# Performance work log

Measured on AMD Instinct MI355X. Metric: run time of the kernel, lower is better.

The kernel has to match this reference:

```python
import jax, jax.numpy as jnp
import numpy as np

NUM_HEADS = 4
NUM_GROUPS = 8
EPS = 1e-5


def setup_inputs() -> dict:
    key = jax.random.key(0)
    ks = jax.random.split(key, 5)
    B, C, H, W = 16, 512, 32, 32
    s = 1.0 / np.sqrt(C)
    return {
        "x": jax.random.normal(ks[0], (B, C, H, W), dtype=jnp.float32),
        "norm_w": jnp.ones((C,), jnp.float32),
        "norm_b": jnp.zeros((C,), jnp.float32),
        "q_w": jax.random.normal(ks[1], (C, C), jnp.float32) * s,
        "q_b": jnp.zeros((C,), jnp.float32),
        "k_w": jax.random.normal(ks[2], (C, C), jnp.float32) * s,
        "k_b": jnp.zeros((C,), jnp.float32),
        "v_w": jax.random.normal(ks[3], (C, C), jnp.float32) * s,
        "v_b": jnp.zeros((C,), jnp.float32),
        "p_w": jax.random.normal(ks[4], (C, C), jnp.float32) * s,
        "p_b": jnp.zeros((C,), jnp.float32),
    }


def _group_norm(x, w, b):
    # x: (B, C, N) -> GroupNorm over (C//G, N) per group
    B, C, N = x.shape
    g = x.reshape(B, NUM_GROUPS, C // NUM_GROUPS, N)
    mean = g.mean(axis=(2, 3), keepdims=True)
    var = g.var(axis=(2, 3), keepdims=True)
    g = (g - mean) * jax.lax.rsqrt(var + EPS)
    x = g.reshape(B, C, N)
    return x * w[None, :, None] + b[None, :, None]


def reference(x, norm_w, norm_b, q_w, q_b, k_w, k_b, v_w, v_b, p_w, p_b):
    B, C, H, W = x.shape
    N = H * W
    Ch = C // NUM_HEADS  # channels per head
    h = _group_norm(x.reshape(B, C, N), norm_w, norm_b)
    # 1x1 Conv1d == channel matmul: (o c, b c n -> b o n)
    q = jnp.einsum('oc,bcn->bon', q_w, h) + q_b[None, :, None]
    k = jnp.einsum('oc,bcn->bon', k_w, h) + k_b[None, :, None]
    v = jnp.einsum('oc,bcn->bon', v_w, h) + v_b[None, :, None]
    q = q.reshape(B, NUM_HEADS, Ch, N)
    k = k.reshape(B, NUM_HEADS, Ch, N)
    v = v.reshape(B, NUM_HEADS, Ch, N)
    attn = jnp.einsum('bhcn,bhcm->bhnm', q, k) * (1.0 / np.sqrt(Ch))
    attn = jax.nn.softmax(attn, axis=-1)
    out = jnp.einsum('bhnm,bhcm->bhcn', attn, v).reshape(B, C, N)
    out = jnp.einsum('oc,bcn->bon', p_w, out) + p_b[None, :, None]
    return x + out.reshape(B, C, H, W)
```

## Files before the change

kernel.cpp:

```cpp
#include <hip/hip_runtime.h>
#include <hip/hip_bf16.h>
#include <math.h>

#define B_    16
#define C_    512
#define N_    1024
#define G_    8
#define HEADS 4
#define CH    128
#define EPS   1e-5f

typedef __attribute__((ext_vector_type(8))) short short8;
typedef __attribute__((ext_vector_type(4))) float f32x4;
typedef __attribute__((ext_vector_type(16))) float f32x16;
typedef __attribute__((ext_vector_type(4))) int i32x4;

__device__ __forceinline__ unsigned short f2bf(float f) {
  union { float f; unsigned int i; } x; x.f = f;
  unsigned int r = x.i + 0x7FFFu + ((x.i >> 16) & 1u);
  return (unsigned short)(r >> 16);
}

__global__ __launch_bounds__(256) void gn_stats(const float* __restrict__ x,
                                                float* __restrict__ stats) {
  int bg = blockIdx.x;
  const float4* p4 = (const float4*)(x + (size_t)bg * (C_ / G_) * N_);
  const int n4 = (C_ / G_) * N_ / 4;
  float s = 0.f, ss = 0.f;
  for (int i = threadIdx.x; i < n4; i += 256) {
    float4 v = p4[i];
    s  += v.x + v.y + v.z + v.w;
    ss += v.x * v.x + v.y * v.y + v.z * v.z + v.w * v.w;
  }
  for (int o = 32; o; o >>= 1) { s += __shfl_down(s, o); ss += __shfl_down(ss, o); }
  __shared__ float ls[4], lss[4];
  int wid = threadIdx.x >> 6, lane = threadIdx.x & 63;
  if (lane == 0) { ls[wid] = s; lss[wid] = ss; }
  __syncthreads();
  if (threadIdx.x == 0) {
    float S = ls[0] + ls[1] + ls[2] + ls[3];
    float SS = lss[0] + lss[1] + lss[2] + lss[3];
    const float inv = 1.f / ((C_ / G_) * N_);
    float mean = S * inv;
    float var = SS * inv - mean * mean;
    stats[bg * 2]     = mean;
    stats[bg * 2 + 1] = rsqrtf(var + EPS);
  }
}

__global__ __launch_bounds__(256) void conv_w(const float* __restrict__ q, const float* __restrict__ k,
                                              const float* __restrict__ v, const float* __restrict__ p,
                                              unsigned short* __restrict__ dst) {
  const int n = C_ * C_;
  int i = blockIdx.x * 256 + threadIdx.x;
  if (i < n) {
    dst[i]         = f2bf(q[i]);
    dst[n + i]     = f2bf(k[i]);
    dst[2 * n + i] = f2bf(v[i]);
    dst[3 * n + i] = f2bf(p[i]);
  }
}

__global__ __launch_bounds__(256) void gn_apply(const float* __restrict__ x,
                                                const float* __restrict__ stats,
                                                const float* __restrict__ gw,
                                                const float* __restrict__ gb,
                                                unsigned short* __restrict__ hT) {
  __shared__ float T[64][65];
  int b = blockIdx.z, c0 = blockIdx.y * 64, n0 = blockIdx.x * 64;
  int g = c0 / (C_ / G_);
  float mean = stats[(b * G_ + g) * 2], rstd = stats[(b * G_ + g) * 2 + 1];
  int t = threadIdx.x;
  for (int it = 0; it < 4; it++) {
    int L = it * 256 + t;
    int cc = L >> 4, nf = L & 15;
    float4 v = *(const float4*)&x[((size_t)b * C_ + c0 + cc) * N_ + n0 + nf * 4];
    float sw = gw[c0 + cc] * rstd, sb = gb[c0 + cc] - mean * sw;
    T[cc][nf * 4 + 0] = v.x * sw + sb;
    T[cc][nf * 4 + 1] = v.y * sw + sb;
    T[cc][nf * 4 + 2] = v.z * sw + sb;
    T[cc][nf * 4 + 3] = v.w * sw + sb;
  }
  __syncthreads();
  for (int it = 0; it < 4; it++) {
    int L = it * 256 + t;
    int nn = L >> 4, cv = L & 15;
    ushort4 o;
    o.x = f2bf(T[cv * 4 + 0][nn]);
    o.y = f2bf(T[cv * 4 + 1][nn]);
    o.z = f2bf(T[cv * 4 + 2][nn]);
    o.w = f2bf(T[cv * 4 + 3][nn]);
    *(ushort4*)&hT[((size_t)b * N_ + n0 + nn) * C_ + c0 + cv * 4] = o;
  }
}

template <bool OUT_BF16, bool BIAS_I, bool RESID>
__global__ __launch_bounds__(256) void gemm_tn(const unsigned short* __restrict__ A,
                                               const unsigned short* __restrict__ Bt,
                                               const float* __restrict__ bias,
                                               const float* __restrict__ resid,
                                               void* __restrict__ out,
                                               int M, int Ncols, int K,
                                               long aBS, long bBS, long oBS) {
  __shared__ __align__(16) unsigned short As[128][72];
  __shared__ __align__(16) unsigned short Bs[128][72];
  int b = blockIdx.z;
  const unsigned short* Ab = A + (size_t)b * aBS;
  const unsigned short* Bb = Bt + (size_t)b * bBS;
  int i0 = blockIdx.y * 128, j0 = blockIdx.x * 128;
  int t = threadIdx.x;
  int w = t >> 6, l = t & 63;
  int wi = (w >> 1) * 64, wj = (w & 1) * 64;
  int lr = l & 15, lk = (l >> 4) * 8;

  f32x4 acc[4][4];
  const f32x4 zf = {0.f, 0.f, 0.f, 0.f};
#pragma unroll
  for (int m = 0; m < 4; m++)
#pragma unroll
    for (int n = 0; n < 4; n++) acc[m][n] = zf;

  for (int kt = 0; kt < K; kt += 64) {
    __syncthreads();
#pragma unroll
    for (int it = 0; it < 4; it++) {
      int L = it * 256 + t;
      int row = L >> 3, c8 = (L & 7) * 8;
      *(uint4*)&As[row][c8] = *(const uint4*)&Ab[(size_t)(i0 + row) * K + kt + c8];
      *(uint4*)&Bs[row][c8] = *(const uint4*)&Bb[(size_t)(j0 + row) * K + kt + c8];
    }
    __syncthreads();
#pragma unroll
    for (int ks = 0; ks < 64; ks += 32) {
      short8 af[4], bf[4];
#pragma unroll
      for (int m = 0; m < 4; m++) af[m] = *(const short8*)&As[wi + m * 16 + lr][ks + lk];
#pragma unroll
      for (int n = 0; n < 4; n++) bf[n] = *(const short8*)&Bs[wj + n * 16 + lr][ks + lk];
#pragma unroll
      for (int m = 0; m < 4; m++)
#pragma unroll
        for (int n = 0; n < 4; n++)
          acc[m][n] = __builtin_amdgcn_mfma_f32_16x16x32_bf16(af[m], bf[n], acc[m][n], 0, 0, 0);
    }
  }

  int rbase = (l >> 4) * 4;
#pragma unroll
  for (int m = 0; m < 4; m++) {
    int ig = i0 + wi + m * 16 + rbase;
#pragma unroll
    for (int n = 0; n < 4; n++) {
      int jg = j0 + wj + n * 16 + lr;
#pragma unroll
      for (int r = 0; r < 4; r++) {
        float vv = acc[m][n][r];
        vv += BIAS_I ? bias[ig + r] : bias[jg];
        size_t oidx = (size_t)b * oBS + (size_t)(ig + r) * Ncols + jg;
        if (RESID) vv += resid[oidx];
        if (OUT_BF16) ((unsigned short*)out)[oidx] = f2bf(vv);
        else ((float*)out)[oidx] = vv;
      }
    }
  }
}

__global__ __launch_bounds__(512, 2) void attn_kernel(const unsigned short* __restrict__ qT,
                                                      const unsigned short* __restrict__ kT,
                                                      const unsigned short* __restrict__ v,
                                                      unsigned short* __restrict__ aoT) {
  __shared__ __align__(16) unsigned short Ks[2][64 * 128];
  __shared__ __align__(16) unsigned short Vs[2][128 * 64];
  const int t = threadIdx.x, w = t >> 6, l = t & 63;
  const int h = l >> 5, l31 = l & 31, l7 = l & 7;
  const int bh = blockIdx.y, b = bh >> 2, hd = bh & 3, c0h = hd * CH;
  const int qg = blockIdx.x * 256 + w * 32 + l31;
  const float sc2 = 0.08838834764831845f * 1.4426950408889634f;
  const float THRRAW = 11.5f / sc2;

  short8 qf[8];
  const unsigned short* qrow = qT + ((size_t)b * N_ + qg) * C_ + c0h;
#pragma unroll
  for (int kc = 0; kc < 8; kc++)
    qf[kc] = *(const short8*)&qrow[kc * 16 + h * 8];

  f32x16 o[4];
#pragma unroll
  for (int ct = 0; ct < 4; ct++) o[ct] = (f32x16)(0.f);
  float m = -INFINITY, lsum = 0.f;

  auto stage = [&](int cur, int tt) {
    int mt = tt * 64;
#pragma unroll
    for (int i = 0; i < 2; i++) {
      int seg = w * 2 + i;
      {
        int row = seg * 4 + (l >> 4);
        int gc = (l & 15) ^ (row & 7);
        const unsigned short* src = kT + ((size_t)b * N_ + mt + row) * C_ + c0h + gc * 8;
        __builtin_amdgcn_global_load_lds((const __attribute__((address_space(1))) void*)src,
                                         (__attribute__((address_space(3))) void*)&Ks[cur][seg * 512],
                                         16, 0, 0);
      }
      {
        int row = seg * 8 + (l >> 3);
        int gc = (l & 7) ^ (row & 7);
        const unsigned short* src = v + ((size_t)b * C_ + c0h + row) * N_ + mt + gc * 8;
        __builtin_amdgcn_global_load_lds((const __attribute__((address_space(1))) void*)src,
                                         (__attribute__((address_space(3))) void*)&Vs[cur][seg * 512],
                                         16, 0, 0);
      }
    }
  };

  stage(0, 0);

  for (int tt = 0; tt < 16; tt++) {
    int cur = tt & 1;
    __syncthreads();
    if (tt < 15) stage(cur ^ 1, tt + 1);

    f32x16 st0 = (f32x16)(0.f), st1 = (f32x16)(0.f);
    const unsigned short* KsB = &Ks[cur][0];
    __builtin_amdgcn_s_setprio(1);
#pragma unroll
    for (int kc = 0; kc < 8; kc++) {
      short8 kf0 = *(const short8*)&KsB[l31 * 128 + (((2 * kc + h) ^ l7) * 8)];
      short8 kf1 = *(const short8*)&KsB[(32 + l31) * 128 + (((2 * kc + h) ^ l7) * 8)];
      st0 = __builtin_amdgcn_mfma_f32_32x32x16_bf16(kf0, qf[kc], st0, 0, 0, 0);
      st1 = __builtin_amdgcn_mfma_f32_32x32x16_bf16(kf1, qf[kc], st1, 0, 0, 0);
    }
    __builtin_amdgcn_s_setprio(0);

    float pmax = st0[0];
#pragma unroll
    for (int r = 1; r < 16; r++) pmax = fmaxf(pmax, st0[r]);
#pragma unroll
    for (int r = 0; r < 16; r++) pmax = fmaxf(pmax, st1[r]);
    pmax = fmaxf(pmax, __shfl_xor(pmax, 32));

    bool defer = (pmax <= m + THRRAW);
    bool skip = __all(defer);
    float mnew = skip ? m : fmaxf(m, pmax);
    float alpha = skip ? 1.f : exp2f((m - mnew) * sc2);
    float mb = mnew * sc2;
    m = mnew;

    float ps = 0.f;
    short8 pf[4];
#pragma unroll
    for (int g = 0; g < 4; g++) {
      const int e0 = (g & 1) * 8;
      float p0, p1, p2, p3, p4, p5, p6, p7;
      if (g < 2) {
        p0 = exp2f(fmaf(st0[e0 + 0], sc2, -mb)); p1 = exp2f(fmaf(st0[e0 + 1], sc2, -mb));
        p2 = exp2f(fmaf(st0[e0 + 2], sc2, -mb)); p3 = exp2f(fmaf(st0[e0 + 3], sc2, -mb));
        p4 = exp2f(fmaf(st0[e0 + 4], sc2, -mb)); p5 = exp2f(fmaf(st0[e0 + 5], sc2, -mb));
        p6 = exp2f(fmaf(st0[e0 + 6], sc2, -mb)); p7 = exp2f(fmaf(st0[e0 + 7], sc2, -mb));
      } else {
        p0 = exp2f(fmaf(st1[e0 + 0], sc2, -mb)); p1 = exp2f(fmaf(st1[e0 + 1], sc2, -mb));
        p2 = exp2f(fmaf(st1[e0 + 2], sc2, -mb)); p3 = exp2f(fmaf(st1[e0 + 3], sc2, -mb));
        p4 = exp2f(fmaf(st1[e0 + 4], sc2, -mb)); p5 = exp2f(fmaf(st1[e0 + 5], sc2, -mb));
        p6 = exp2f(fmaf(st1[e0 + 6], sc2, -mb)); p7 = exp2f(fmaf(st1[e0 + 7], sc2, -mb));
      }
      ps += p0 + p1 + p2 + p3 + p4 + p5 + p6 + p7;
      unsigned int x, x2, y, y2;
      asm("v_cvt_pk_bf16_f32 %0, %1, %2" : "=v"(x)  : "v"(p0), "v"(p1));
      asm("v_cvt_pk_bf16_f32 %0, %1, %2" : "=v"(x2) : "v"(p2), "v"(p3));
      asm("v_cvt_pk_bf16_f32 %0, %1, %2" : "=v"(y)  : "v"(p4), "v"(p5));
      asm("v_cvt_pk_bf16_f32 %0, %1, %2" : "=v"(y2) : "v"(p6), "v"(p7));
      asm("v_permlane32_swap_b32 %0, %1" : "+v"(x), "+v"(y));
      asm("v_permlane32_swap_b32 %0, %1" : "+v"(x2), "+v"(y2));
      i32x4 pwv = {(int)x, (int)x2, (int)y, (int)y2};
      pf[g] = __builtin_bit_cast(short8, pwv);
    }
    ps += __shfl_xor(ps, 32);
    lsum = lsum * alpha + ps;

    if (!skip) {
#pragma unroll
      for (int ct = 0; ct < 4; ct++)
#pragma unroll
        for (int r = 0; r < 16; r++) o[ct][r] *= alpha;
    }

    const unsigned short* VsB = &Vs[cur][0];
    __builtin_amdgcn_s_setprio(1);
#pragma unroll
    for (int ct = 0; ct < 4; ct++) {
#pragma unroll
      for (int g = 0; g < 4; g++) {
        short8 vf = *(const short8*)&VsB[(ct * 32 + l31) * 64 + (((2 * g + h) ^ l7) * 8)];
        o[ct] = __builtin_amdgcn_mfma_f32_32x32x16_bf16(vf, pf[g], o[ct], 0, 0, 0);
      }
    }
    __builtin_amdgcn_s_setprio(0);
  }

  float rn = 1.f / lsum;
  unsigned short* orow = aoT + ((size_t)b * N_ + qg) * C_ + c0h;
#pragma unroll
  for (int ct = 0; ct < 4; ct++)
#pragma unroll
    for (int u = 0; u < 4; u++) {
      ushort4 ov;
      ov.x = f2bf(o[ct][u * 4 + 0] * rn);
      ov.y = f2bf(o[ct][u * 4 + 1] * rn);
      ov.z = f2bf(o[ct][u * 4 + 2] * rn);
      ov.w = f2bf(o[ct][u * 4 + 3] * rn);
      *(ushort4*)&orow[ct * 32 + u * 8 + h * 4] = ov;
    }
}

extern "C" void kernel_launch(void* const* d_in, const int* in_sizes, int n_in,
                              void* d_out, int out_size, void* d_ws, size_t ws_size,
                              hipStream_t stream) {
  const float* x  = (const float*)d_in[0];
  const float* nw = (const float*)d_in[1];
  const float* nb = (const float*)d_in[2];
  const float* qw = (const float*)d_in[3];
  const float* qb = (const float*)d_in[4];
  const float* kw = (const float*)d_in[5];
  const float* kb = (const float*)d_in[6];
  const float* vw = (const float*)d_in[7];
  const float* vb = (const float*)d_in[8];
  const float* pw = (const float*)d_in[9];
  const float* pb = (const float*)d_in[10];

  char* ws = (char*)d_ws;
  unsigned short* wbf  = (unsigned short*)ws;
  float*          stats = (float*)(ws + 0x200000);
  unsigned short* hT   = (unsigned short*)(ws + 0x201000);
  unsigned short* qT   = (unsigned short*)(ws + 0x1201000);
  unsigned short* kT   = (unsigned short*)(ws + 0x2201000);
  unsigned short* vv   = (unsigned short*)(ws + 0x3201000);
  unsigned short* aoT  = hT;

  const long NC = (long)N_ * C_;
  const int n_w = C_ * C_;

  gn_stats<<<B_ * G_, 256, 0, stream>>>(x, stats);
  conv_w<<<n_w / 256, 256, 0, stream>>>(qw, kw, vw, pw, wbf);
  gn_apply<<<dim3(N_ / 64, C_ / 64, B_), 256, 0, stream>>>(x, stats, nw, nb, hT);

  gemm_tn<true, false, false><<<dim3(C_ / 128, N_ / 128, B_), 256, 0, stream>>>(
      hT, wbf, qb, nullptr, qT, N_, C_, C_, NC, 0, NC);
  gemm_tn<true, false, false><<<dim3(C_ / 128, N_ / 128, B_), 256, 0, stream>>>(
      hT, wbf + n_w, kb, nullptr, kT, N_, C_, C_, NC, 0, NC);
  gemm_tn<true, true, false><<<dim3(N_ / 128, C_ / 128, B_), 256, 0, stream>>>(
      wbf + 2 * n_w, hT, vb, nullptr, vv, C_, N_, C_, 0, NC, NC);

  attn_kernel<<<dim3(N_ / 256, B_ * HEADS), 512, 0, stream>>>(qT, kT, vv, aoT);

  gemm_tn<false, true, true><<<dim3(N_ / 128, C_ / 128, B_), 256, 0, stream>>>(
      wbf + 3 * n_w, aoT, pb, x, d_out, C_, N_, C_, 0, NC, NC);
}
```

Baseline: 160.7 us.

## Fuse Q/K projections, use direct-to-LDS loads in GEMM, shrink attention blocks

```diff
diff --git a/kernel.cpp b/kernel.cpp
--- a/kernel.cpp
+++ b/kernel.cpp
@@ -50,7 +50,9 @@
 
 __global__ __launch_bounds__(256) void conv_w(const float* __restrict__ q, const float* __restrict__ k,
                                               const float* __restrict__ v, const float* __restrict__ p,
-                                              unsigned short* __restrict__ dst) {
+                                              const float* __restrict__ qb, const float* __restrict__ kb,
+                                              unsigned short* __restrict__ dst,
+                                              float* __restrict__ qkb) {
   const int n = C_ * C_;
   int i = blockIdx.x * 256 + threadIdx.x;
   if (i < n) {
@@ -59,6 +61,7 @@
     dst[2 * n + i] = f2bf(v[i]);
     dst[3 * n + i] = f2bf(p[i]);
   }
+  if (i < 1024) qkb[i] = (i < 512) ? qb[i] : kb[i - 512];
 }
 
 __global__ __launch_bounds__(256) void gn_apply(const float* __restrict__ x,
@@ -100,18 +103,18 @@
                                                const float* __restrict__ bias,
                                                const float* __restrict__ resid,
                                                void* __restrict__ out,
-                                               int M, int Ncols, int K,
+                                               int Ncols, int K,
                                                long aBS, long bBS, long oBS) {
-  __shared__ __align__(16) unsigned short As[128][72];
-  __shared__ __align__(16) unsigned short Bs[128][72];
-  int b = blockIdx.z;
-  const unsigned short* Ab = A + (size_t)b * aBS;
-  const unsigned short* Bb = Bt + (size_t)b * bBS;
-  int i0 = blockIdx.y * 128, j0 = blockIdx.x * 128;
-  int t = threadIdx.x;
-  int w = t >> 6, l = t & 63;
-  int wi = (w >> 1) * 64, wj = (w & 1) * 64;
-  int lr = l & 15, lk = (l >> 4) * 8;
+  __shared__ __align__(16) unsigned short As[128 * 64];
+  __shared__ __align__(16) unsigned short Bs[128 * 64];
+  const int b = blockIdx.z;
+  const int i0 = blockIdx.y * 128, j0 = blockIdx.x * 128;
+  const unsigned short* Ab = A + (size_t)b * aBS + (size_t)i0 * K;
+  const unsigned short* Bb = Bt + (size_t)b * bBS + (size_t)j0 * K;
+  const int t = threadIdx.x, w = t >> 6, l = t & 63;
+  const int wi = (w >> 1) * 64, wj = (w & 1) * 64;
+  const int lr = l & 15, lk = (l >> 4) * 8;
+  const int srow = l >> 3, scol = (l & 7) * 8;
 
   f32x4 acc[4][4];
   const f32x4 zf = {0.f, 0.f, 0.f, 0.f};
@@ -123,20 +126,24 @@
   for (int kt = 0; kt < K; kt += 64) {
     __syncthreads();
 #pragma unroll
-    for (int it = 0; it < 4; it++) {
-      int L = it * 256 + t;
-      int row = L >> 3, c8 = (L & 7) * 8;
-      *(uint4*)&As[row][c8] = *(const uint4*)&Ab[(size_t)(i0 + row) * K + kt + c8];
-      *(uint4*)&Bs[row][c8] = *(const uint4*)&Bb[(size_t)(j0 + row) * K + kt + c8];
+    for (int i = 0; i < 4; i++) {
+      int seg = w * 4 + i;
+      int row = seg * 8 + srow;
+      __builtin_amdgcn_global_load_lds(
+          (const __attribute__((address_space(1))) void*)&Ab[(size_t)row * K + kt + scol],
+          (__attribute__((address_space(3))) void*)&As[seg * 512], 16, 0, 0);
+      __builtin_amdgcn_global_load_lds(
+          (const __attribute__((address_space(1))) void*)&Bb[(size_t)row * K + kt + scol],
+          (__attribute__((address_space(3))) void*)&Bs[seg * 512], 16, 0, 0);
     }
     __syncthreads();
 #pragma unroll
     for (int ks = 0; ks < 64; ks += 32) {
       short8 af[4], bf[4];
 #pragma unroll
-      for (int m = 0; m < 4; m++) af[m] = *(const short8*)&As[wi + m * 16 + lr][ks + lk];
-#pragma unroll
-      for (int n = 0; n < 4; n++) bf[n] = *(const short8*)&Bs[wj + n * 16 + lr][ks + lk];
+      for (int m = 0; m < 4; m++) af[m] = *(const short8*)&As[(wi + m * 16 + lr) * 64 + ks + lk];
+#pragma unroll
+      for (int n = 0; n < 4; n++) bf[n] = *(const short8*)&Bs[(wj + n * 16 + lr) * 64 + ks + lk];
 #pragma unroll
       for (int m = 0; m < 4; m++)
 #pragma unroll
@@ -165,8 +172,7 @@
   }
 }
 
-__global__ __launch_bounds__(512, 2) void attn_kernel(const unsigned short* __restrict__ qT,
-                                                      const unsigned short* __restrict__ kT,
+__global__ __launch_bounds__(256, 2) void attn_kernel(const unsigned short* __restrict__ qkT,
                                                       const unsigned short* __restrict__ v,
                                                       unsigned short* __restrict__ aoT) {
   __shared__ __align__(16) unsigned short Ks[2][64 * 128];
@@ -174,12 +180,12 @@
   const int t = threadIdx.x, w = t >> 6, l = t & 63;
   const int h = l >> 5, l31 = l & 31, l7 = l & 7;
   const int bh = blockIdx.y, b = bh >> 2, hd = bh & 3, c0h = hd * CH;
-  const int qg = blockIdx.x * 256 + w * 32 + l31;
+  const int qg = blockIdx.x * 128 + w * 32 + l31;
   const float sc2 = 0.08838834764831845f * 1.4426950408889634f;
   const float THRRAW = 11.5f / sc2;
 
   short8 qf[8];
-  const unsigned short* qrow = qT + ((size_t)b * N_ + qg) * C_ + c0h;
+  const unsigned short* qrow = qkT + ((size_t)b * N_ + qg) * 1024 + c0h;
 #pragma unroll
   for (int kc = 0; kc < 8; kc++)
     qf[kc] = *(const short8*)&qrow[kc * 16 + h * 8];
@@ -192,12 +198,12 @@
   auto stage = [&](int cur, int tt) {
     int mt = tt * 64;
 #pragma unroll
-    for (int i = 0; i < 2; i++) {
-      int seg = w * 2 + i;
+    for (int i = 0; i < 4; i++) {
+      int seg = w * 4 + i;
       {
         int row = seg * 4 + (l >> 4);
         int gc = (l & 15) ^ (row & 7);
-        const unsigned short* src = kT + ((size_t)b * N_ + mt + row) * C_ + c0h + gc * 8;
+        const unsigned short* src = qkT + ((size_t)b * N_ + mt + row) * 1024 + 512 + c0h + gc * 8;
         __builtin_amdgcn_global_load_lds((const __attribute__((address_space(1))) void*)src,
                                          (__attribute__((address_space(3))) void*)&Ks[cur][seg * 512],
                                          16, 0, 0);
@@ -232,12 +238,14 @@
     }
     __builtin_amdgcn_s_setprio(0);
 
-    float pmax = st0[0];
-#pragma unroll
-    for (int r = 1; r < 16; r++) pmax = fmaxf(pmax, st0[r]);
-#pragma unroll
-    for (int r = 0; r < 16; r++) pmax = fmaxf(pmax, st1[r]);
-    pmax = fmaxf(pmax, __shfl_xor(pmax, 32));
+    float tr[16];
+#pragma unroll
+    for (int r = 0; r < 16; r++) tr[r] = fmaxf(st0[r], st1[r]);
+#pragma unroll
+    for (int s = 8; s >= 1; s >>= 1)
+#pragma unroll
+      for (int r = 0; r < s; r++) tr[r] = fmaxf(tr[r], tr[r + s]);
+    float pmax = fmaxf(tr[0], __shfl_xor(tr[0], 32));
 
     bool defer = (pmax <= m + THRRAW);
     bool skip = __all(defer);
@@ -246,7 +254,7 @@
     float mb = mnew * sc2;
     m = mnew;
 
-    float ps = 0.f;
+    float psg[4];
     short8 pf[4];
 #pragma unroll
     for (int g = 0; g < 4; g++) {
@@ -263,7 +271,8 @@
         p4 = exp2f(fmaf(st1[e0 + 4], sc2, -mb)); p5 = exp2f(fmaf(st1[e0 + 5], sc2, -mb));
         p6 = exp2f(fmaf(st1[e0 + 6], sc2, -mb)); p7 = exp2f(fmaf(st1[e0 + 7], sc2, -mb));
       }
-      ps += p0 + p1 + p2 + p3 + p4 + p5 + p6 + p7;
+      float s01 = p0 + p1, s23 = p2 + p3, s45 = p4 + p5, s67 = p6 + p7;
+      psg[g] = (s01 + s23) + (s45 + s67);
       unsigned int x, x2, y, y2;
       asm("v_cvt_pk_bf16_f32 %0, %1, %2" : "=v"(x)  : "v"(p0), "v"(p1));
       asm("v_cvt_pk_bf16_f32 %0, %1, %2" : "=v"(x2) : "v"(p2), "v"(p3));
@@ -274,6 +283,7 @@
       i32x4 pwv = {(int)x, (int)x2, (int)y, (int)y2};
       pf[g] = __builtin_bit_cast(short8, pwv);
     }
+    float ps = (psg[0] + psg[1]) + (psg[2] + psg[3]);
     ps += __shfl_xor(ps, 32);
     lsum = lsum * alpha + ps;
 
@@ -330,9 +340,9 @@
   char* ws = (char*)d_ws;
   unsigned short* wbf  = (unsigned short*)ws;
   float*          stats = (float*)(ws + 0x200000);
+  float*          qkb  = (float*)(ws + 0x200800);
   unsigned short* hT   = (unsigned short*)(ws + 0x201000);
-  unsigned short* qT   = (unsigned short*)(ws + 0x1201000);
-  unsigned short* kT   = (unsigned short*)(ws + 0x2201000);
+  unsigned short* qkT  = (unsigned short*)(ws + 0x1201000);
   unsigned short* vv   = (unsigned short*)(ws + 0x3201000);
   unsigned short* aoT  = hT;
 
@@ -340,18 +350,16 @@
   const int n_w = C_ * C_;
 
   gn_stats<<<B_ * G_, 256, 0, stream>>>(x, stats);
-  conv_w<<<n_w / 256, 256, 0, stream>>>(qw, kw, vw, pw, wbf);
+  conv_w<<<n_w / 256, 256, 0, stream>>>(qw, kw, vw, pw, qb, kb, wbf, qkb);
   gn_apply<<<dim3(N_ / 64, C_ / 64, B_), 256, 0, stream>>>(x, stats, nw, nb, hT);
 
-  gemm_tn<true, false, false><<<dim3(C_ / 128, N_ / 128, B_), 256, 0, stream>>>(
-      hT, wbf, qb, nullptr, qT, N_, C_, C_, NC, 0, NC);
-  gemm_tn<true, false, false><<<dim3(C_ / 128, N_ / 128, B_), 256, 0, stream>>>(
-      hT, wbf + n_w, kb, nullptr, kT, N_, C_, C_, NC, 0, NC);
+  gemm_tn<true, false, false><<<dim3(1024 / 128, N_ / 128, B_), 256, 0, stream>>>(
+      hT, wbf, qkb, nullptr, qkT, 1024, C_, NC, 0, (long)N_ * 1024);
   gemm_tn<true, true, false><<<dim3(N_ / 128, C_ / 128, B_), 256, 0, stream>>>(
-      wbf + 2 * n_w, hT, vb, nullptr, vv, C_, N_, C_, 0, NC, NC);
-
-  attn_kernel<<<dim3(N_ / 256, B_ * HEADS), 512, 0, stream>>>(qT, kT, vv, aoT);
+      wbf + 2 * n_w, hT, vb, nullptr, vv, N_, C_, 0, NC, NC);
+
+  attn_kernel<<<dim3(N_ / 128, B_ * HEADS), 256, 0, stream>>>(qkT, vv, aoT);
 
   gemm_tn<false, true, true><<<dim3(N_ / 128, C_ / 128, B_), 256, 0, stream>>>(
-      wbf + 3 * n_w, aoT, pb, x, d_out, C_, N_, C_, 0, NC, NC);
-}
+      wbf + 3 * n_w, aoT, pb, x, d_out, N_, C_, 0, NC, NC);
+}
```

After: 165.8 us. +3.2%, slower.
